# Optimization experiments

Hardware: AMD Instinct MI355X
Metric: run time of the kernel (lower is better)

The kernel has to match this reference:

```python
import jax, jax.numpy as jnp
import numpy as np

EMBED_DIM = 1024
NUM_HEADS = 16
HEAD_DIM = EMBED_DIM // NUM_HEADS
RANK = 512
B, S = 4, 4096


def setup_inputs() -> dict:
    key = jax.random.key(0)
    ks = jax.random.split(key, 16)
    sd = 0.02
    inp = {
        "query": jax.random.normal(ks[0], (B, S, EMBED_DIM), jnp.float32),
        "key": jax.random.normal(ks[1], (B, S, EMBED_DIM), jnp.float32),
        "value": jax.random.normal(ks[2], (B, S, EMBED_DIM), jnp.float32),
        # torch nn.Linear weights: [out_features, in_features]
        "q_down_w": jax.random.normal(ks[3], (RANK, EMBED_DIM), jnp.float32) * sd,
        "q_up_w": jax.random.normal(ks[4], (EMBED_DIM, RANK), jnp.float32) * sd,
        "q_up_b": jax.random.normal(ks[5], (EMBED_DIM,), jnp.float32) * sd,
        "k_down_w": jax.random.normal(ks[6], (RANK, EMBED_DIM), jnp.float32) * sd,
        "k_up_w": jax.random.normal(ks[7], (EMBED_DIM, RANK), jnp.float32) * sd,
        "k_up_b": jax.random.normal(ks[8], (EMBED_DIM,), jnp.float32) * sd,
        "v_down_w": jax.random.normal(ks[9], (RANK, EMBED_DIM), jnp.float32) * sd,
        "v_up_w": jax.random.normal(ks[10], (EMBED_DIM, RANK), jnp.float32) * sd,
        "v_up_b": jax.random.normal(ks[11], (EMBED_DIM,), jnp.float32) * sd,
        "out_w": jax.random.normal(ks[12], (EMBED_DIM, EMBED_DIM), jnp.float32) * sd,
        "out_b": jax.random.normal(ks[13], (EMBED_DIM,), jnp.float32) * sd,
    }
    return inp


def _linear(x, w, b=None):
    y = x @ w.T
    return y if b is None else y + b


def reference(query, key, value,
              q_down_w, q_up_w, q_up_b,
              k_down_w, k_up_w, k_up_b,
              v_down_w, v_up_w, v_up_b,
              out_w, out_b):
    b, s, _ = query.shape
    # low-rank QKV projections
    q = _linear(_linear(query, q_down_w), q_up_w, q_up_b)
    k = _linear(_linear(key, k_down_w), k_up_w, k_up_b)
    v = _linear(_linear(value, v_down_w), v_up_w, v_up_b)
    # [B,S,E] -> [B,H,S,Dh]
    q = q.reshape(b, s, NUM_HEADS, HEAD_DIM).transpose(0, 2, 1, 3)
    k = k.reshape(b, s, NUM_HEADS, HEAD_DIM).transpose(0, 2, 1, 3)
    v = v.reshape(b, s, NUM_HEADS, HEAD_DIM).transpose(0, 2, 1, 3)
    # kernel feature map: elu + 1  (note: scaling_factor in original is computed but unused)
    q = jax.nn.elu(q) + 1.0
    k = jax.nn.elu(k) + 1.0
    k_sum = k.sum(axis=-2)                              # [B,H,Dh]
    denom = jnp.einsum('bhnd,bhd->bhn', q, k_sum)       # [B,H,S]
    kv = jnp.einsum('bhnd,bhne->bhde', k, v)            # [B,H,Dh,Dh]
    num = jnp.einsum('bhnd,bhde->bhne', q, kv)          # [B,H,S,Dh]
    out = num / (denom[..., None] + 1e-6)
    out = out.transpose(0, 2, 1, 3).reshape(b, s, EMBED_DIM)
    return _linear(out, out_w, out_b)
```

## Files before the change

kernel.cpp:

```cpp
#include <hip/hip_runtime.h>
#include <hip/hip_bf16.h>

typedef unsigned short ushort_t;
typedef unsigned int uint_t;
typedef __attribute__((ext_vector_type(8))) short short8;
typedef __attribute__((ext_vector_type(4))) float f32x4;

#define EMBED 1024
#define RANK  512
#define BB    4
#define SS    4096
#define HH    16
#define DHD   64
#define MM    (BB*SS)
#define NCHUNK 16

__device__ __forceinline__ float bf2f(ushort_t u) {
    union { uint_t i; float f; } v; v.i = ((uint_t)u) << 16; return v.f;
}
__device__ __forceinline__ ushort_t f2bf(float f) {
    union { float f; uint_t i; } v; v.f = f;
    uint_t r = v.i + 0x7FFFu + ((v.i >> 16) & 1u);
    return (ushort_t)(r >> 16);
}
__device__ __forceinline__ void gl2lds16(const void* g, void* l) {
    __builtin_amdgcn_global_load_lds((const __attribute__((address_space(1))) void*)g,
                                     (__attribute__((address_space(3))) void*)l,
                                     16, 0, 0);
}

template<int EPI, int AF32>
__global__ __launch_bounds__(256) void gemm_bt(
    const void* __restrict__ A0, const void* __restrict__ A1, const void* __restrict__ A2,
    const ushort_t* __restrict__ B0, const ushort_t* __restrict__ B1, const ushort_t* __restrict__ B2,
    const float* __restrict__ bias0, const float* __restrict__ bias1, const float* __restrict__ bias2,
    void* __restrict__ C0, void* __restrict__ C1, void* __restrict__ C2,
    int N, int K, int nbx)
{
    __shared__ __align__(16) ushort_t As[128 * 32];
    __shared__ __align__(16) ushort_t Bs[128 * 32];

    const int z = blockIdx.z;
    const void*     Av   = (z == 0) ? A0 : (z == 1) ? A1 : A2;
    const ushort_t* Bm   = (z == 0) ? B0 : (z == 1) ? B1 : B2;
    const float*    bias = (z == 0) ? bias0 : (z == 1) ? bias1 : bias2;
    void*           Cv   = (z == 0) ? C0 : (z == 1) ? C1 : C2;

    const int cpx = gridDim.x >> 3;
    const int bid = blockIdx.x;
    const int wg  = (bid & 7) * cpx + (bid >> 3);
    const long m0 = (long)(wg / nbx) * 128;
    const long n0 = (long)(wg % nbx) * 128;

    const int t = threadIdx.x;
    const int lane = t & 63;
    const int w = t >> 6;
    const int wr = (w >> 1) * 64;
    const int wc = (w & 1) * 64;
    const int fr = lane & 15;
    const int kq = (lane >> 4) * 8;

    f32x4 acc[4][4] = {};

    const ushort_t* Ab = (const ushort_t*)Av;
    const float*    Af = (const float*)Av;
    const int srow = t >> 2;
    const int scol = (t & 3) * 8;

    for (int k0 = 0; k0 < K; k0 += 32) {
        if (AF32) {
            #pragma unroll
            for (int r = 0; r < 2; ++r) {
                const int row = srow + r * 64;
                const float* src = Af + (m0 + row) * (long)K + k0 + scol;
                f32x4 f0 = *(const f32x4*)src;
                f32x4 f1 = *(const f32x4*)(src + 4);
                short8 h;
                h[0] = (short)f2bf(f0[0]); h[1] = (short)f2bf(f0[1]);
                h[2] = (short)f2bf(f0[2]); h[3] = (short)f2bf(f0[3]);
                h[4] = (short)f2bf(f1[0]); h[5] = (short)f2bf(f1[1]);
                h[6] = (short)f2bf(f1[2]); h[7] = (short)f2bf(f1[3]);
                *(short8*)&As[row * 32 + scol] = h;
            }
        } else {
            #pragma unroll
            for (int ro = 0; ro < 2; ++ro) {
                const int idx = ro * 256 + t;
                const int row = idx >> 2;
                const int c8 = (idx & 3) * 8;
                gl2lds16(Ab + (m0 + row) * (long)K + k0 + c8,
                         (char*)As + (ro * 256 + w * 64) * 16);
            }
        }
        #pragma unroll
        for (int ro = 0; ro < 2; ++ro) {
            const int idx = ro * 256 + t;
            const int row = idx >> 2;
            const int c8 = (idx & 3) * 8;
            gl2lds16(Bm + (n0 + row) * (long)K + k0 + c8,
                     (char*)Bs + (ro * 256 + w * 64) * 16);
        }
        __syncthreads();

        short8 av[4], bv[4];
        #pragma unroll
        for (int mi = 0; mi < 4; ++mi)
            av[mi] = *(const short8*)&As[(wr + mi * 16 + fr) * 32 + kq];
        #pragma unroll
        for (int nf = 0; nf < 4; ++nf)
            bv[nf] = *(const short8*)&Bs[(wc + nf * 16 + fr) * 32 + kq];
        #pragma unroll
        for (int mi = 0; mi < 4; ++mi)
            #pragma unroll
            for (int nf = 0; nf < 4; ++nf)
                acc[mi][nf] = __builtin_amdgcn_mfma_f32_16x16x32_bf16(
                    av[mi], bv[nf], acc[mi][nf], 0, 0, 0);
        __syncthreads();
    }

    ushort_t* Cb = (ushort_t*)Cv;
    float*    Cf = (float*)Cv;
    const int rj = (lane >> 4) * 4;
    const bool do_elu = (EPI == 2) && (z < 2);
    #pragma unroll
    for (int nf = 0; nf < 4; ++nf) {
        const long col = n0 + wc + nf * 16 + fr;
        const float bval = (EPI >= 1) ? bias[col] : 0.0f;
        #pragma unroll
        for (int mi = 0; mi < 4; ++mi) {
            #pragma unroll
            for (int j = 0; j < 4; ++j) {
                const long row = m0 + wr + mi * 16 + rj + j;
                float x = acc[mi][nf][j];
                if (EPI >= 1) x += bval;
                if (do_elu) x = (x > 0.0f) ? (x + 1.0f) : __expf(x);
                if (EPI == 3) Cf[row * (long)N + col] = x;
                else          Cb[row * (long)N + col] = f2bf(x);
            }
        }
    }
}

__global__ __launch_bounds__(256) void kv_stats(const ushort_t* __restrict__ Kp,
                                                const ushort_t* __restrict__ Vp,
                                                float* __restrict__ kvp,
                                                float* __restrict__ ksump)
{
    __shared__ __align__(16) ushort_t Ks[64 * 64];
    __shared__ __align__(16) ushort_t Vs[64 * 64];
    const int t = threadIdx.x;
    const int w = t >> 6;
    const int bh = blockIdx.x;
    const int chunk = blockIdx.y;
    const int b = bh >> 4, h = bh & 15;
    const int d0 = (t & 15) * 4;
    const int e0 = (t >> 4) * 4;
    float acc[4][4] = {};
    float sks[4] = {};
    const long hbase = ((long)b * SS) * EMBED + h * DHD;

    for (int sub = 0; sub < 4; ++sub) {
        const int n00 = chunk * 256 + sub * 64;
        #pragma unroll
        for (int ro = 0; ro < 2; ++ro) {
            const int idx = ro * 256 + t;
            const int r = idx >> 3, c16 = idx & 7;
            const long g = hbase + (long)(n00 + r) * EMBED + c16 * 8;
            gl2lds16(Kp + g, (char*)Ks + (ro * 256 + w * 64) * 16);
            gl2lds16(Vp + g, (char*)Vs + (ro * 256 + w * 64) * 16);
        }
        __syncthreads();
        #pragma unroll 8
        for (int n = 0; n < 64; ++n) {
            const uint_t* kr = (const uint_t*)(Ks + n * 64 + d0);
            const uint_t* vr = (const uint_t*)(Vs + n * 64 + e0);
            const uint_t k01 = kr[0], k23 = kr[1];
            const uint_t v01 = vr[0], v23 = vr[1];
            float kd[4], ve[4];
            {
                union { uint_t i; float f; } a, bq, c, dq;
                a.i = k01 << 16; bq.i = k01 & 0xffff0000u;
                c.i = k23 << 16; dq.i = k23 & 0xffff0000u;
                kd[0] = a.f; kd[1] = bq.f; kd[2] = c.f; kd[3] = dq.f;
            }
            {
                union { uint_t i; float f; } a, bq, c, dq;
                a.i = v01 << 16; bq.i = v01 & 0xffff0000u;
                c.i = v23 << 16; dq.i = v23 & 0xffff0000u;
                ve[0] = a.f; ve[1] = bq.f; ve[2] = c.f; ve[3] = dq.f;
            }
            #pragma unroll
            for (int e = 0; e < 4; ++e)
                #pragma unroll
                for (int d = 0; d < 4; ++d)
                    acc[e][d] += ve[e] * kd[d];
            if (e0 == 0) {
                #pragma unroll
                for (int d = 0; d < 4; ++d) sks[d] += kd[d];
            }
        }
        __syncthreads();
    }

    float* dst = kvp + ((long)chunk * 64 + bh) * 4096;
    #pragma unroll
    for (int e = 0; e < 4; ++e) {
        f32x4 vv; vv[0] = acc[e][0]; vv[1] = acc[e][1]; vv[2] = acc[e][2]; vv[3] = acc[e][3];
        *(f32x4*)(dst + (e0 + e) * 64 + d0) = vv;
    }
    if (e0 == 0) {
        float* sd = ksump + ((long)chunk * 64 + bh) * 64 + d0;
        #pragma unroll
        for (int d = 0; d < 4; ++d) sd[d] = sks[d];
    }
}

__global__ __launch_bounds__(256) void kv_reduce(const float* __restrict__ kvp,
                                                 const float* __restrict__ ksump,
                                                 ushort_t* __restrict__ kvb,
                                                 float* __restrict__ ksumf)
{
    const int bh = blockIdx.x;
    const int t = threadIdx.x;
    const long base = (long)bh * 4096 + t * 16;
    f32x4 s[4] = {};
    #pragma unroll 4
    for (int c = 0; c < NCHUNK; ++c) {
        const float* src = kvp + (long)c * 64 * 4096 + base;
        #pragma unroll
        for (int j = 0; j < 4; ++j) s[j] += *(const f32x4*)(src + j * 4);
    }
    short8 o0, o1;
    #pragma unroll
    for (int j = 0; j < 4; ++j) {
        o0[j]     = (short)f2bf(s[0][j]); o0[4 + j] = (short)f2bf(s[1][j]);
        o1[j]     = (short)f2bf(s[2][j]); o1[4 + j] = (short)f2bf(s[3][j]);
    }
    *(short8*)(kvb + base)     = o0;
    *(short8*)(kvb + base + 8) = o1;

    if (t < 64) {
        float ss = 0.f;
        #pragma unroll
        for (int c = 0; c < NCHUNK; ++c) ss += ksump[(long)c * 64 * 64 + bh * 64 + t];
        ksumf[bh * 64 + t] = ss;
    }
}

__global__ __launch_bounds__(256) void cvt_weights(
    const float* __restrict__ s0, const float* __restrict__ s1,
    const float* __restrict__ s2, const float* __restrict__ s3,
    const float* __restrict__ s4, const float* __restrict__ s5,
    const float* __restrict__ s6,
    ushort_t* __restrict__ d0, ushort_t* __restrict__ d1,
    ushort_t* __restrict__ d2, ushort_t* __restrict__ d3,
    ushort_t* __restrict__ d4, ushort_t* __restrict__ d5,
    ushort_t* __restrict__ d6)
{
    const int y = blockIdx.y;
    const float* src; ushort_t* dst; int n;
    switch (y) {
        case 0: src = s0; dst = d0; n = RANK * EMBED; break;
        case 1: src = s1; dst = d1; n = RANK * EMBED; break;
        case 2: src = s2; dst = d2; n = RANK * EMBED; break;
        case 3: src = s3; dst = d3; n = RANK * EMBED; break;
        case 4: src = s4; dst = d4; n = RANK * EMBED; break;
        case 5: src = s5; dst = d5; n = RANK * EMBED; break;
        default: src = s6; dst = d6; n = EMBED * EMBED; break;
    }
    const int i = (blockIdx.x * 256 + threadIdx.x) * 4;
    if (i < n) {
        f32x4 f = *(const f32x4*)(src + i);
        typedef __attribute__((ext_vector_type(4))) short short4v;
        short4v h;
        h[0] = (short)f2bf(f[0]); h[1] = (short)f2bf(f[1]);
        h[2] = (short)f2bf(f[2]); h[3] = (short)f2bf(f[3]);
        *(short4v*)(dst + i) = h;
    }
}

__global__ __launch_bounds__(256) void attn_out(const ushort_t* __restrict__ Qp,
                                                const ushort_t* __restrict__ kvb,
                                                const float* __restrict__ ksum,
                                                ushort_t* __restrict__ Op)
{
    __shared__ __align__(16) ushort_t Qs[128 * 64];
    __shared__ __align__(16) ushort_t KVs[64 * 64];
    __shared__ float kss[64];
    __shared__ float dnm[128];
    const int t = threadIdx.x;
    const int w = t >> 6, lane = t & 63;
    const int bh = blockIdx.x, mc = blockIdx.y;
    const int b = bh >> 4, h = bh & 15;
    const long base = ((long)b * SS + mc * 128) * EMBED + h * DHD;

    #pragma unroll
    for (int ro = 0; ro < 4; ++ro) {
        const int idx = ro * 256 + t;
        const int r = idx >> 3, c16 = idx & 7;
        gl2lds16(Qp + base + (long)r * EMBED + c16 * 8,
                 (char*)Qs + (ro * 256 + w * 64) * 16);
    }
    #pragma unroll
    for (int ro = 0; ro < 2; ++ro) {
        const int idx = ro * 256 + t;
        gl2lds16(kvb + (long)bh * 4096 + idx * 8,
                 (char*)KVs + (ro * 256 + w * 64) * 16);
    }
    if (t < 64) kss[t] = ksum[bh * 64 + t];
    __syncthreads();

    if (t < 128) {
        float s = 0.f;
        const uint_t* qr = (const uint_t*)(Qs + t * 64);
        #pragma unroll
        for (int jj = 0; jj < 32; ++jj) {
            const uint_t u = qr[jj];
            union { uint_t i; float f; } lo, hi;
            lo.i = u << 16; hi.i = u & 0xffff0000u;
            s += lo.f * kss[2 * jj] + hi.f * kss[2 * jj + 1];
        }
        dnm[t] = s;
    }

    const int fr = lane & 15, kq = (lane >> 4) * 8;
    f32x4 acc[2][4] = {};
    #pragma unroll
    for (int ks = 0; ks < 2; ++ks) {
        short8 av[2], bv[4];
        #pragma unroll
        for (int mi = 0; mi < 2; ++mi)
            av[mi] = *(const short8*)&Qs[(w * 32 + mi * 16 + fr) * 64 + ks * 32 + kq];
        #pragma unroll
        for (int nf = 0; nf < 4; ++nf)
            bv[nf] = *(const short8*)&KVs[(nf * 16 + fr) * 64 + ks * 32 + kq];
        #pragma unroll
        for (int mi = 0; mi < 2; ++mi)
            #pragma unroll
            for (int nf = 0; nf < 4; ++nf)
                acc[mi][nf] = __builtin_amdgcn_mfma_f32_16x16x32_bf16(
                    av[mi], bv[nf], acc[mi][nf], 0, 0, 0);
    }
    __syncthreads();

    const int rj = (lane >> 4) * 4;
    #pragma unroll
    for (int mi = 0; mi < 2; ++mi) {
        #pragma unroll
        for (int nf = 0; nf < 4; ++nf) {
            #pragma unroll
            for (int j = 0; j < 4; ++j) {
                const int r = w * 32 + mi * 16 + rj + j;
                const int c = nf * 16 + fr;
                const float x = acc[mi][nf][j] / (dnm[r] + 1e-6f);
                Op[base + (long)r * EMBED + c] = f2bf(x);
            }
        }
    }
}

extern "C" void kernel_launch(void* const* d_in, const int* in_sizes, int n_in,
                              void* d_out, int out_size, void* d_ws, size_t ws_size,
                              hipStream_t stream)
{
    (void)in_sizes; (void)n_in; (void)out_size; (void)ws_size;
    const float* query = (const float*)d_in[0];
    const float* key_  = (const float*)d_in[1];
    const float* value = (const float*)d_in[2];
    const float* q_dw  = (const float*)d_in[3];
    const float* q_uw  = (const float*)d_in[4];
    const float* q_ub  = (const float*)d_in[5];
    const float* k_dw  = (const float*)d_in[6];
    const float* k_uw  = (const float*)d_in[7];
    const float* k_ub  = (const float*)d_in[8];
    const float* v_dw  = (const float*)d_in[9];
    const float* v_uw  = (const float*)d_in[10];
    const float* v_ub  = (const float*)d_in[11];
    const float* o_w   = (const float*)d_in[12];
    const float* o_b   = (const float*)d_in[13];

    char* ws = (char*)d_ws;
    size_t off = 0;
    auto alloc = [&](size_t bytes) -> void* {
        void* p = ws + off;
        off += (bytes + 255) & ~(size_t)255;
        return p;
    };
    const size_t WSMALL = (size_t)RANK * EMBED;
    ushort_t* bw_qd = (ushort_t*)alloc(WSMALL * 2);
    ushort_t* bw_qu = (ushort_t*)alloc(WSMALL * 2);
    ushort_t* bw_kd = (ushort_t*)alloc(WSMALL * 2);
    ushort_t* bw_ku = (ushort_t*)alloc(WSMALL * 2);
    ushort_t* bw_vd = (ushort_t*)alloc(WSMALL * 2);
    ushort_t* bw_vu = (ushort_t*)alloc(WSMALL * 2);
    ushort_t* bw_o  = (ushort_t*)alloc((size_t)EMBED * EMBED * 2);
    ushort_t* Y1q   = (ushort_t*)alloc((size_t)MM * RANK * 2);
    ushort_t* Y1k   = (ushort_t*)alloc((size_t)MM * RANK * 2);
    ushort_t* Y1v   = (ushort_t*)alloc((size_t)MM * RANK * 2);
    ushort_t* PQ    = (ushort_t*)alloc((size_t)MM * EMBED * 2);
    ushort_t* PK    = (ushort_t*)alloc((size_t)MM * EMBED * 2);
    ushort_t* PV    = (ushort_t*)alloc((size_t)MM * EMBED * 2);
    float*    ksump = (float*)alloc((size_t)NCHUNK * 64 * 64 * 4);
    float*    ksumf = (float*)alloc((size_t)64 * 64 * 4);
    ushort_t* kvb   = (ushort_t*)alloc((size_t)64 * 64 * 64 * 2);
    ushort_t* O     = (ushort_t*)alloc((size_t)MM * EMBED * 2);

    float* kvp = (float*)Y1q;

    const dim3 blk(256);

    cvt_weights<<<dim3(EMBED * EMBED / 1024, 7), blk, 0, stream>>>(
        q_dw, q_uw, k_dw, k_uw, v_dw, v_uw, o_w,
        bw_qd, bw_qu, bw_kd, bw_ku, bw_vd, bw_vu, bw_o);

    gemm_bt<0, 1><<<dim3(MM / 128 * (RANK / 128), 1, 3), blk, 0, stream>>>(
        query, key_, value,
        bw_qd, bw_kd, bw_vd,
        nullptr, nullptr, nullptr,
        Y1q, Y1k, Y1v,
        RANK, EMBED, RANK / 128);

    gemm_bt<2, 0><<<dim3(MM / 128 * (EMBED / 128), 1, 3), blk, 0, stream>>>(
        Y1q, Y1k, Y1v,
        bw_qu, bw_ku, bw_vu,
        q_ub, k_ub, v_ub,
        PQ, PK, PV,
        EMBED, RANK, EMBED / 128);

    kv_stats<<<dim3(64, NCHUNK), blk, 0, stream>>>(PK, PV, kvp, ksump);
    kv_reduce<<<dim3(64), blk, 0, stream>>>(kvp, ksump, kvb, ksumf);
    attn_out<<<dim3(64, 32), blk, 0, stream>>>(PQ, kvb, ksumf, O);

    gemm_bt<3, 0><<<dim3(MM / 128 * (EMBED / 128), 1, 1), blk, 0, stream>>>(
        O, nullptr, nullptr,
        bw_o, nullptr, nullptr,
        o_b, nullptr, nullptr,
        d_out, nullptr, nullptr,
        EMBED, EMBED, EMBED / 128);
}
```

Before: 331.8 us.

## Double-buffer GEMM LDS tiles and pre-convert activations to bf16

The GEMM now double-buffers its A and B LDS tiles. It issues async global_load_lds for the next K-slice while MFMAs run on the current one, with one barrier per iteration. The fp32-to-bf16 conversion of query, key and value moves from the first GEMM's load path into a separate cvt_act pass, so every GEMM can use the async LDS load path. This costs an extra full read and write of the input activations. Workspace buffers are aliased so the converted inputs, and later the projections and attention output, reuse memory.

```diff
diff --git a/kernel.cpp b/kernel.cpp
--- a/kernel.cpp
+++ b/kernel.cpp
@@ -29,19 +29,19 @@
                                      16, 0, 0);
 }
 
-template<int EPI, int AF32>
+template<int EPI>
 __global__ __launch_bounds__(256) void gemm_bt(
-    const void* __restrict__ A0, const void* __restrict__ A1, const void* __restrict__ A2,
+    const ushort_t* __restrict__ A0, const ushort_t* __restrict__ A1, const ushort_t* __restrict__ A2,
     const ushort_t* __restrict__ B0, const ushort_t* __restrict__ B1, const ushort_t* __restrict__ B2,
     const float* __restrict__ bias0, const float* __restrict__ bias1, const float* __restrict__ bias2,
     void* __restrict__ C0, void* __restrict__ C1, void* __restrict__ C2,
     int N, int K, int nbx)
 {
-    __shared__ __align__(16) ushort_t As[128 * 32];
-    __shared__ __align__(16) ushort_t Bs[128 * 32];
+    __shared__ __align__(16) ushort_t As[2][128 * 32];
+    __shared__ __align__(16) ushort_t Bs[2][128 * 32];
 
     const int z = blockIdx.z;
-    const void*     Av   = (z == 0) ? A0 : (z == 1) ? A1 : A2;
+    const ushort_t* Ab   = (z == 0) ? A0 : (z == 1) ? A1 : A2;
     const ushort_t* Bm   = (z == 0) ? B0 : (z == 1) ? B1 : B2;
     const float*    bias = (z == 0) ? bias0 : (z == 1) ? bias1 : bias2;
     void*           Cv   = (z == 0) ? C0 : (z == 1) ? C1 : C2;
@@ -60,62 +60,46 @@
     const int fr = lane & 15;
     const int kq = (lane >> 4) * 8;
 
-    f32x4 acc[4][4] = {};
-
-    const ushort_t* Ab = (const ushort_t*)Av;
-    const float*    Af = (const float*)Av;
     const int srow = t >> 2;
     const int scol = (t & 3) * 8;
 
-    for (int k0 = 0; k0 < K; k0 += 32) {
-        if (AF32) {
-            #pragma unroll
-            for (int r = 0; r < 2; ++r) {
-                const int row = srow + r * 64;
-                const float* src = Af + (m0 + row) * (long)K + k0 + scol;
-                f32x4 f0 = *(const f32x4*)src;
-                f32x4 f1 = *(const f32x4*)(src + 4);
-                short8 h;
-                h[0] = (short)f2bf(f0[0]); h[1] = (short)f2bf(f0[1]);
-                h[2] = (short)f2bf(f0[2]); h[3] = (short)f2bf(f0[3]);
-                h[4] = (short)f2bf(f1[0]); h[5] = (short)f2bf(f1[1]);
-                h[6] = (short)f2bf(f1[2]); h[7] = (short)f2bf(f1[3]);
-                *(short8*)&As[row * 32 + scol] = h;
-            }
-        } else {
-            #pragma unroll
-            for (int ro = 0; ro < 2; ++ro) {
-                const int idx = ro * 256 + t;
-                const int row = idx >> 2;
-                const int c8 = (idx & 3) * 8;
-                gl2lds16(Ab + (m0 + row) * (long)K + k0 + c8,
-                         (char*)As + (ro * 256 + w * 64) * 16);
-            }
-        }
+    f32x4 acc[4][4] = {};
+
+    auto STAGE = [&](int k0, int buf) {
         #pragma unroll
         for (int ro = 0; ro < 2; ++ro) {
-            const int idx = ro * 256 + t;
-            const int row = idx >> 2;
-            const int c8 = (idx & 3) * 8;
-            gl2lds16(Bm + (n0 + row) * (long)K + k0 + c8,
-                     (char*)Bs + (ro * 256 + w * 64) * 16);
-        }
-        __syncthreads();
+            const int row = ro * 64 + srow;
+            gl2lds16(Ab + (m0 + row) * (long)K + k0 + scol,
+                     (char*)As[buf] + (ro * 256 + w * 64) * 16);
+            gl2lds16(Bm + (n0 + row) * (long)K + k0 + scol,
+                     (char*)Bs[buf] + (ro * 256 + w * 64) * 16);
+        }
+    };
+
+    STAGE(0, 0);
+    __syncthreads();
+
+    int cur = 0;
+    const int nt = K >> 5;
+    for (int ti = 0; ti < nt; ++ti) {
+        if (ti + 1 < nt) STAGE((ti + 1) << 5, cur ^ 1);
 
         short8 av[4], bv[4];
         #pragma unroll
         for (int mi = 0; mi < 4; ++mi)
-            av[mi] = *(const short8*)&As[(wr + mi * 16 + fr) * 32 + kq];
+            av[mi] = *(const short8*)&As[cur][(wr + mi * 16 + fr) * 32 + kq];
         #pragma unroll
         for (int nf = 0; nf < 4; ++nf)
-            bv[nf] = *(const short8*)&Bs[(wc + nf * 16 + fr) * 32 + kq];
+            bv[nf] = *(const short8*)&Bs[cur][(wc + nf * 16 + fr) * 32 + kq];
         #pragma unroll
         for (int mi = 0; mi < 4; ++mi)
             #pragma unroll
             for (int nf = 0; nf < 4; ++nf)
                 acc[mi][nf] = __builtin_amdgcn_mfma_f32_16x16x32_bf16(
                     av[mi], bv[nf], acc[mi][nf], 0, 0, 0);
+
         __syncthreads();
+        cur ^= 1;
     }
 
     ushort_t* Cb = (ushort_t*)Cv;
@@ -125,19 +109,72 @@
     #pragma unroll
     for (int nf = 0; nf < 4; ++nf) {
         const long col = n0 + wc + nf * 16 + fr;
-        const float bval = (EPI >= 1) ? bias[col] : 0.0f;
+        const float bval = (EPI >= 2) ? bias[col] : 0.0f;
         #pragma unroll
         for (int mi = 0; mi < 4; ++mi) {
             #pragma unroll
             for (int j = 0; j < 4; ++j) {
                 const long row = m0 + wr + mi * 16 + rj + j;
                 float x = acc[mi][nf][j];
-                if (EPI >= 1) x += bval;
+                if (EPI >= 2) x += bval;
                 if (do_elu) x = (x > 0.0f) ? (x + 1.0f) : __expf(x);
                 if (EPI == 3) Cf[row * (long)N + col] = x;
                 else          Cb[row * (long)N + col] = f2bf(x);
             }
         }
+    }
+}
+
+__global__ __launch_bounds__(256) void cvt_act(const float* __restrict__ q,
+                                               const float* __restrict__ k,
+                                               const float* __restrict__ v,
+                                               ushort_t* __restrict__ qo,
+                                               ushort_t* __restrict__ ko,
+                                               ushort_t* __restrict__ vo)
+{
+    const int zz = blockIdx.y;
+    const float* src = (zz == 0) ? q : (zz == 1) ? k : v;
+    ushort_t*    dst = (zz == 0) ? qo : (zz == 1) ? ko : vo;
+    const long i = ((long)blockIdx.x * 256 + threadIdx.x) * 8;
+    f32x4 f0 = *(const f32x4*)(src + i);
+    f32x4 f1 = *(const f32x4*)(src + i + 4);
+    short8 h;
+    h[0] = (short)f2bf(f0[0]); h[1] = (short)f2bf(f0[1]);
+    h[2] = (short)f2bf(f0[2]); h[3] = (short)f2bf(f0[3]);
+    h[4] = (short)f2bf(f1[0]); h[5] = (short)f2bf(f1[1]);
+    h[6] = (short)f2bf(f1[2]); h[7] = (short)f2bf(f1[3]);
+    *(short8*)(dst + i) = h;
+}
+
+__global__ __launch_bounds__(256) void cvt_weights(
+    const float* __restrict__ s0, const float* __restrict__ s1,
+    const float* __restrict__ s2, const float* __restrict__ s3,
+    const float* __restrict__ s4, const float* __restrict__ s5,
+    const float* __restrict__ s6,
+    ushort_t* __restrict__ d0, ushort_t* __restrict__ d1,
+    ushort_t* __restrict__ d2, ushort_t* __restrict__ d3,
+    ushort_t* __restrict__ d4, ushort_t* __restrict__ d5,
+    ushort_t* __restrict__ d6)
+{
+    const int y = blockIdx.y;
+    const float* src; ushort_t* dst; int n;
+    switch (y) {
+        case 0: src = s0; dst = d0; n = RANK * EMBED; break;
+        case 1: src = s1; dst = d1; n = RANK * EMBED; break;
+        case 2: src = s2; dst = d2; n = RANK * EMBED; break;
+        case 3: src = s3; dst = d3; n = RANK * EMBED; break;
+        case 4: src = s4; dst = d4; n = RANK * EMBED; break;
+        case 5: src = s5; dst = d5; n = RANK * EMBED; break;
+        default: src = s6; dst = d6; n = EMBED * EMBED; break;
+    }
+    const int i = (blockIdx.x * 256 + threadIdx.x) * 4;
+    if (i < n) {
+        f32x4 f = *(const f32x4*)(src + i);
+        typedef __attribute__((ext_vector_type(4))) short short4v;
+        short4v h;
+        h[0] = (short)f2bf(f[0]); h[1] = (short)f2bf(f[1]);
+        h[2] = (short)f2bf(f[2]); h[3] = (short)f2bf(f[3]);
+        *(short4v*)(dst + i) = h;
     }
 }
 
@@ -247,38 +284,6 @@
     }
 }
 
-__global__ __launch_bounds__(256) void cvt_weights(
-    const float* __restrict__ s0, const float* __restrict__ s1,
-    const float* __restrict__ s2, const float* __restrict__ s3,
-    const float* __restrict__ s4, const float* __restrict__ s5,
-    const float* __restrict__ s6,
-    ushort_t* __restrict__ d0, ushort_t* __restrict__ d1,
-    ushort_t* __restrict__ d2, ushort_t* __restrict__ d3,
-    ushort_t* __restrict__ d4, ushort_t* __restrict__ d5,
-    ushort_t* __restrict__ d6)
-{
-    const int y = blockIdx.y;
-    const float* src; ushort_t* dst; int n;
-    switch (y) {
-        case 0: src = s0; dst = d0; n = RANK * EMBED; break;
-        case 1: src = s1; dst = d1; n = RANK * EMBED; break;
-        case 2: src = s2; dst = d2; n = RANK * EMBED; break;
-        case 3: src = s3; dst = d3; n = RANK * EMBED; break;
-        case 4: src = s4; dst = d4; n = RANK * EMBED; break;
-        case 5: src = s5; dst = d5; n = RANK * EMBED; break;
-        default: src = s6; dst = d6; n = EMBED * EMBED; break;
-    }
-    const int i = (blockIdx.x * 256 + threadIdx.x) * 4;
-    if (i < n) {
-        f32x4 f = *(const f32x4*)(src + i);
-        typedef __attribute__((ext_vector_type(4))) short short4v;
-        short4v h;
-        h[0] = (short)f2bf(f[0]); h[1] = (short)f2bf(f[1]);
-        h[2] = (short)f2bf(f[2]); h[3] = (short)f2bf(f[3]);
-        *(short4v*)(dst + i) = h;
-    }
-}
-
 __global__ __launch_bounds__(256) void attn_out(const ushort_t* __restrict__ Qp,
                                                 const ushort_t* __restrict__ kvb,
                                                 const float* __restrict__ ksum,
@@ -394,33 +399,38 @@
     ushort_t* bw_vd = (ushort_t*)alloc(WSMALL * 2);
     ushort_t* bw_vu = (ushort_t*)alloc(WSMALL * 2);
     ushort_t* bw_o  = (ushort_t*)alloc((size_t)EMBED * EMBED * 2);
+    ushort_t* Qb    = (ushort_t*)alloc((size_t)MM * EMBED * 2);
+    ushort_t* Kb    = (ushort_t*)alloc((size_t)MM * EMBED * 2);
+    ushort_t* Vb    = (ushort_t*)alloc((size_t)MM * EMBED * 2);
     ushort_t* Y1q   = (ushort_t*)alloc((size_t)MM * RANK * 2);
     ushort_t* Y1k   = (ushort_t*)alloc((size_t)MM * RANK * 2);
     ushort_t* Y1v   = (ushort_t*)alloc((size_t)MM * RANK * 2);
-    ushort_t* PQ    = (ushort_t*)alloc((size_t)MM * EMBED * 2);
-    ushort_t* PK    = (ushort_t*)alloc((size_t)MM * EMBED * 2);
-    ushort_t* PV    = (ushort_t*)alloc((size_t)MM * EMBED * 2);
     float*    ksump = (float*)alloc((size_t)NCHUNK * 64 * 64 * 4);
     float*    ksumf = (float*)alloc((size_t)64 * 64 * 4);
     ushort_t* kvb   = (ushort_t*)alloc((size_t)64 * 64 * 64 * 2);
-    ushort_t* O     = (ushort_t*)alloc((size_t)MM * EMBED * 2);
-
-    float* kvp = (float*)Y1q;
+
+    ushort_t* PQ = Qb;
+    ushort_t* PK = Kb;
+    ushort_t* PV = Vb;
+    float*    kvp = (float*)Y1q;
+    ushort_t* O   = Y1k;
 
     const dim3 blk(256);
 
+    cvt_act<<<dim3((size_t)MM * EMBED / 2048, 3), blk, 0, stream>>>(
+        query, key_, value, Qb, Kb, Vb);
     cvt_weights<<<dim3(EMBED * EMBED / 1024, 7), blk, 0, stream>>>(
         q_dw, q_uw, k_dw, k_uw, v_dw, v_uw, o_w,
         bw_qd, bw_qu, bw_kd, bw_ku, bw_vd, bw_vu, bw_o);
 
-    gemm_bt<0, 1><<<dim3(MM / 128 * (RANK / 128), 1, 3), blk, 0, stream>>>(
-        query, key_, value,
+    gemm_bt<0><<<dim3(MM / 128 * (RANK / 128), 1, 3), blk, 0, stream>>>(
+        Qb, Kb, Vb,
         bw_qd, bw_kd, bw_vd,
         nullptr, nullptr, nullptr,
         Y1q, Y1k, Y1v,
         RANK, EMBED, RANK / 128);
 
-    gemm_bt<2, 0><<<dim3(MM / 128 * (EMBED / 128), 1, 3), blk, 0, stream>>>(
+    gemm_bt<2><<<dim3(MM / 128 * (EMBED / 128), 1, 3), blk, 0, stream>>>(
         Y1q, Y1k, Y1v,
         bw_qu, bw_ku, bw_vu,
         q_ub, k_ub, v_ub,
@@ -431,7 +441,7 @@
     kv_reduce<<<dim3(64), blk, 0, stream>>>(kvp, ksump, kvb, ksumf);
     attn_out<<<dim3(64, 32), blk, 0, stream>>>(PQ, kvb, ksumf, O);
 
-    gemm_bt<3, 0><<<dim3(MM / 128 * (EMBED / 128), 1, 1), blk, 0, stream>>>(
+    gemm_bt<3><<<dim3(MM / 128 * (EMBED / 128), 1, 1), blk, 0, stream>>>(
         O, nullptr, nullptr,
         bw_o, nullptr, nullptr,
         o_b, nullptr, nullptr,
```

Result: no change. 329.9 us (-0.6%).
